# Performance work log

Measured on AMD Instinct MI355X. Metric: run time of the kernel, lower is better.

The kernel has to match this reference:

```python
import jax, jax.numpy as jnp
import numpy as np

D_MODEL = 768
N_HEAD = 12


def setup_inputs() -> dict:
    key = jax.random.key(0)
    k1, k2, k3, k4, k5 = jax.random.split(key, 5)
    B, T, C = 4, 2048, D_MODEL
    s = 1.0 / np.sqrt(C)
    return {
        "x": jax.random.normal(k1, (B, T, C), dtype=jnp.float32),
        "w_attn": jax.random.normal(k2, (C, 3 * C), dtype=jnp.float32) * s,
        "b_attn": jax.random.normal(k3, (3 * C,), dtype=jnp.float32) * 0.02,
        "w_proj": jax.random.normal(k4, (C, C), dtype=jnp.float32) * s,
        "b_proj": jax.random.normal(k5, (C,), dtype=jnp.float32) * 0.02,
    }


def reference(x, w_attn, b_attn, w_proj, b_proj):
    B, T, C = x.shape
    H = N_HEAD
    Dh = C // H
    qkv = x @ w_attn + b_attn                      # [B, T, 3C]
    q, k, v = jnp.split(qkv, 3, axis=-1)
    # [B, H, T, Dh]
    q = q.reshape(B, T, H, Dh).transpose(0, 2, 1, 3)
    k = k.reshape(B, T, H, Dh).transpose(0, 2, 1, 3)
    v = v.reshape(B, T, H, Dh).transpose(0, 2, 1, 3)
    att = jnp.einsum("bhqd,bhkd->bhqk", q, k) * (1.0 / np.sqrt(Dh))
    causal = jnp.tril(jnp.ones((T, T), dtype=bool))
    att = jnp.where(causal[None, None, :, :], att, -jnp.inf)
    att = jax.nn.softmax(att, axis=-1)             # dropout p=0 (eval)
    y = jnp.einsum("bhqk,bhkd->bhqd", att, v)      # [B, H, T, Dh]
    y = y.transpose(0, 2, 1, 3).reshape(B, T, C)
    return y @ w_proj + b_proj
```

## Files before the change

### kernel.cpp

```cpp
#include <hip/hip_runtime.h>
#include <stdint.h>

#define NHEAD 12
#define DH 64
#define BATCH 4
#define SEQ 2048
#define CDIM 768
#define MROWS (BATCH*SEQ)

typedef __attribute__((ext_vector_type(8))) short short8;
typedef __attribute__((ext_vector_type(4))) float floatx4;
typedef unsigned int u32;

__device__ inline unsigned short f2bf(float f) {
    union { float f; unsigned u; } v; v.f = f;
    unsigned r = v.u + 0x7FFFu + ((v.u >> 16) & 1u);
    return (unsigned short)(r >> 16);
}

__device__ __forceinline__ u32 pk_bf16(float a, float b) {
    u32 d;
    asm("v_cvt_pk_bf16_f32 %0, %1, %2" : "=v"(d) : "v"(a), "v"(b));
    return d;
}

__device__ __forceinline__ void async_cp16(const unsigned short* g, unsigned short* l) {
    __builtin_amdgcn_global_load_lds(
        (const __attribute__((address_space(1))) u32*)g,
        (__attribute__((address_space(3))) u32*)l, 16, 0, 0);
}

__global__ void convert_f32_bf16(const float* __restrict__ in,
                                 unsigned short* __restrict__ out, int n) {
    int i = (blockIdx.x * blockDim.x + threadIdx.x) * 4;
    if (i + 3 < n) {
        float4 f = *(const float4*)(in + i);
        union { unsigned short s[4]; uint2 u; } p;
        p.s[0] = f2bf(f.x); p.s[1] = f2bf(f.y);
        p.s[2] = f2bf(f.z); p.s[3] = f2bf(f.w);
        *(uint2*)(out + i) = p.u;
    }
}

__global__ __launch_bounds__(256) void transpose_conv(
    const float* __restrict__ in, unsigned short* __restrict__ out,
    int K, int N) {
    __shared__ unsigned short T[64][72];
    const int k0 = blockIdx.x * 64, n0 = blockIdx.y * 64;
    const int t = threadIdx.x;
    const int nc = t & 63, kw = t >> 6;
    for (int i = 0; i < 16; i++) {
        const int kr = kw + i * 4;
        T[nc][kr] = f2bf(in[(size_t)(k0 + kr) * N + n0 + nc]);
    }
    __syncthreads();
    const int row = t >> 2, seg = t & 3;
    uint4 a = *(const uint4*)&T[row][seg * 16];
    uint4 b2 = *(const uint4*)&T[row][seg * 16 + 8];
    unsigned short* o = &out[(size_t)(n0 + row) * K + k0 + seg * 16];
    *(uint4*)o = a;
    *(uint4*)(o + 8) = b2;
}

template<int MODE>
__global__ __launch_bounds__(256) void gemm_bf16(
    const unsigned short* __restrict__ A,
    const unsigned short* __restrict__ BT,
    const float* __restrict__ bias,
    float* __restrict__ Cout,
    unsigned short* __restrict__ Qout,
    unsigned short* __restrict__ Kout,
    unsigned short* __restrict__ VTout,
    int Ndim, int Kdim)
{
    __shared__ unsigned short As[2][128 * 32];
    __shared__ unsigned short Bs[2][128 * 32];
    const int tid  = threadIdx.x;
    const int wave = tid >> 6;
    const int lane = tid & 63;
    const int l16  = lane & 15;
    const int quad = lane >> 4;
    const int wm = wave >> 1, wn = wave & 1;
    const int m0 = blockIdx.x * 128;
    const int n0 = blockIdx.y * 128;

    const int rloc = lane >> 2;
    const int gs   = ((lane & 3) ^ (rloc & 3) ^ ((rloc >> 2) & 3)) * 8;
    const int ar0  = wave * 32 + rloc;
    const int pg = ((quad ^ (l16 & 3) ^ ((l16 >> 2) & 3))) * 8;

    floatx4 acc[4][4];
    for (int i = 0; i < 4; i++)
        for (int j = 0; j < 4; j++) acc[i][j] = (floatx4)0.0f;

    for (int ch = 0; ch < 2; ch++) {
        const int row = ar0 + ch * 16;
        async_cp16(&A[(size_t)(m0 + row) * Kdim + gs], &As[0][(wave * 2 + ch) * 512]);
        async_cp16(&BT[(size_t)(n0 + row) * Kdim + gs], &Bs[0][(wave * 2 + ch) * 512]);
    }
    __syncthreads();

    for (int k0 = 0; k0 < Kdim; k0 += 32) {
        const int cur = (k0 >> 5) & 1;
        if (k0 + 32 < Kdim) {
            for (int ch = 0; ch < 2; ch++) {
                const int row = ar0 + ch * 16;
                async_cp16(&A[(size_t)(m0 + row) * Kdim + k0 + 32 + gs],
                           &As[cur ^ 1][(wave * 2 + ch) * 512]);
                async_cp16(&BT[(size_t)(n0 + row) * Kdim + k0 + 32 + gs],
                           &Bs[cur ^ 1][(wave * 2 + ch) * 512]);
            }
        }
        short8 a[4], b[4];
        for (int i = 0; i < 4; i++)
            a[i] = *(const short8*)&As[cur][(wm * 64 + i * 16 + l16) * 32 + pg];
        for (int j = 0; j < 4; j++)
            b[j] = *(const short8*)&Bs[cur][(wn * 64 + j * 16 + l16) * 32 + pg];
        for (int i = 0; i < 4; i++)
            for (int j = 0; j < 4; j++)
                acc[i][j] = __builtin_amdgcn_mfma_f32_16x16x32_bf16(
                    a[i], b[j], acc[i][j], 0, 0, 0);
        __syncthreads();
    }

    const float QSCALE = 0.18033688011112042f;
    for (int i = 0; i < 4; i++) {
        const int mbase = m0 + wm * 64 + i * 16 + quad * 4;
        for (int j = 0; j < 4; j++) {
            const int ncol = n0 + wn * 64 + j * 16 + l16;
            const float bv = bias[ncol];
            for (int r = 0; r < 4; r++) {
                const int m = mbase + r;
                const float v = acc[i][j][r] + bv;
                if (MODE == 0) {
                    Cout[(size_t)m * Ndim + ncol] = v;
                } else {
                    const int b_  = m >> 11, t = m & 2047;
                    const int part = ncol / CDIM;
                    const int c = ncol - part * CDIM;
                    const int h = c >> 6, d = c & 63;
                    const size_t bh = (size_t)(b_ * NHEAD + h);
                    if (part == 0)
                        Qout[(bh * SEQ + t) * DH + d] = f2bf(v * QSCALE);
                    else if (part == 1)
                        Kout[(bh * SEQ + t) * DH + d] = f2bf(v);
                    else
                        VTout[(bh * DH + d) * SEQ + t] = f2bf(v);
                }
            }
        }
    }
}

__global__ __launch_bounds__(256) void attn_kernel(
    const unsigned short* __restrict__ Q,
    const unsigned short* __restrict__ K,
    const unsigned short* __restrict__ VT,
    unsigned short* __restrict__ O)
{
    __shared__ unsigned short Kl[2][2][64 * 32];
    __shared__ unsigned short Vl[2][2][64 * 32];
    __shared__ unsigned short Pl[4][16 * 68];

    const int tid  = threadIdx.x;
    const int wave = tid >> 6;
    const int lane = tid & 63;
    const int l16  = lane & 15;
    const int quad = lane >> 4;

    const int lin = blockIdx.x;
    const int grp = lin >> 3;
    const int xs  = grp & 15;
    const int bh  = ((grp >> 4) << 3) | (lin & 7);
    const int h = bh % NHEAD, b = bh / NHEAD;

    const unsigned short* Qp = Q  + (size_t)bh * SEQ * DH;
    const unsigned short* Kp = K  + (size_t)bh * SEQ * DH;
    const unsigned short* Vp = VT + (size_t)bh * DH * SEQ;

    const int rloc = lane >> 2;
    const int gofsK = ((lane & 3) ^ (rloc & 3) ^ ((rloc >> 2) & 3)) * 8;
    const int pg = ((quad ^ (l16 & 3) ^ ((l16 >> 2) & 3))) * 8;

    for (int pass = 0; pass < 2; pass++) {
        const int qtile = pass == 0 ? xs : 31 - xs;
        const int qb = qtile * 64;
        const int qw = qb + wave * 16;
        const int nkt = qtile + 1;

        short8 aq[2];
        for (int c = 0; c < 2; c++)
            aq[c] = *(const short8*)&Qp[(size_t)(qw + l16) * DH + c * 32 + quad * 8];

        floatx4 accO[4];
        for (int dt = 0; dt < 4; dt++) accO[dt] = (floatx4)0.0f;
        float lp = 0.0f;

        {
            const int krow = wave * 16 + rloc;
            for (int c = 0; c < 2; c++) {
                async_cp16(&Kp[(size_t)krow * DH + c * 32 + gofsK],
                           &Kl[0][c][wave * 512]);
                async_cp16(&Vp[(size_t)krow * SEQ + 0 + c * 32 + gofsK],
                           &Vl[0][c][wave * 512]);
            }
        }
        __syncthreads();

        for (int kt = 0; kt < nkt; kt++) {
            const int kb  = kt * 64;
            const int cur = kt & 1;

            if (kt + 1 < nkt) {
                const int kbn = kb + 64;
                const int krow = wave * 16 + rloc;
                for (int c = 0; c < 2; c++) {
                    async_cp16(&Kp[(size_t)(kbn + krow) * DH + c * 32 + gofsK],
                               &Kl[cur ^ 1][c][wave * 512]);
                    async_cp16(&Vp[(size_t)krow * SEQ + kbn + c * 32 + gofsK],
                               &Vl[cur ^ 1][c][wave * 512]);
                }
            }

            floatx4 s[4];
            for (int jn = 0; jn < 4; jn++) {
                s[jn] = (floatx4)0.0f;
                for (int c = 0; c < 2; c++) {
                    short8 bk = *(const short8*)
                        &Kl[cur][c][(jn * 16 + l16) * 32 + pg];
                    s[jn] = __builtin_amdgcn_mfma_f32_16x16x32_bf16(
                        bk, aq[c], s[jn], 0, 0, 0);
                }
            }

            if (kt == nkt - 1) {
                const int q = qw + l16;
                for (int jn = 0; jn < 4; jn++) {
                    const int key = kb + jn * 16 + quad * 4;
                    for (int r = 0; r < 4; r++)
                        if (key + r > q) s[jn][r] = -1e30f;
                }
            }

            for (int jn = 0; jn < 4; jn++)
                for (int r = 0; r < 4; r++) {
                    float p = exp2f(s[jn][r]);
                    s[jn][r] = p;
                    lp += p;
                }

            for (int jn = 0; jn < 4; jn++) {
                uint2 u;
                u.x = pk_bf16(s[jn][0], s[jn][1]);
                u.y = pk_bf16(s[jn][2], s[jn][3]);
                *(uint2*)&Pl[wave][l16 * 68 + jn * 16 + quad * 4] = u;
            }
            short8 ap[2];
            for (int c = 0; c < 2; c++) {
                union { short8 v; uint2 u2[2]; } a_;
                const int base = l16 * 68 + c * 32 + quad * 8;
                a_.u2[0] = *(const uint2*)&Pl[wave][base];
                a_.u2[1] = *(const uint2*)&Pl[wave][base + 4];
                ap[c] = a_.v;
            }

            for (int dt = 0; dt < 4; dt++)
                for (int c = 0; c < 2; c++) {
                    short8 bv = *(const short8*)
                        &Vl[cur][c][(dt * 16 + l16) * 32 + pg];
                    accO[dt] = __builtin_amdgcn_mfma_f32_16x16x32_bf16(
                        ap[c], bv, accO[dt], 0, 0, 0);
                }

            __syncthreads();
        }

        float L = lp;
        L += __shfl_xor(L, 16);
        L += __shfl_xor(L, 32);
        for (int r = 0; r < 4; r++) {
            const float Lr = __shfl(L, (lane & 48) | (quad * 4 + r), 64);
            const float inv = 1.0f / Lr;
            const int t = qb + wave * 16 + quad * 4 + r;
            const size_t base = ((size_t)b * SEQ + t) * CDIM + h * DH;
            for (int dt = 0; dt < 4; dt++)
                O[base + dt * 16 + l16] = f2bf(accO[dt][r] * inv);
        }
        __syncthreads();
    }
}

extern "C" void kernel_launch(void* const* d_in, const int* in_sizes, int n_in,
                              void* d_out, int out_size, void* d_ws, size_t ws_size,
                              hipStream_t stream) {
    const float* x      = (const float*)d_in[0];
    const float* w_attn = (const float*)d_in[1];
    const float* b_attn = (const float*)d_in[2];
    const float* w_proj = (const float*)d_in[3];
    const float* b_proj = (const float*)d_in[4];
    float* out = (float*)d_out;

    unsigned short* xb   = (unsigned short*)d_ws;
    unsigned short* wta  = xb  + (size_t)MROWS * CDIM;
    unsigned short* wtp  = wta + (size_t)3 * CDIM * CDIM;
    unsigned short* qws  = wtp + (size_t)CDIM * CDIM;
    unsigned short* kws  = qws + (size_t)MROWS * CDIM;
    unsigned short* vtws = kws + (size_t)MROWS * CDIM;
    unsigned short* ob   = xb;

    const int nx = MROWS * CDIM;
    convert_f32_bf16<<<nx / 1024, 256, 0, stream>>>(x, xb, nx);
    transpose_conv<<<dim3(CDIM / 64, 3 * CDIM / 64), 256, 0, stream>>>(
        w_attn, wta, CDIM, 3 * CDIM);
    transpose_conv<<<dim3(CDIM / 64, CDIM / 64), 256, 0, stream>>>(
        w_proj, wtp, CDIM, CDIM);

    dim3 g1(MROWS / 128, (3 * CDIM) / 128);
    gemm_bf16<1><<<g1, 256, 0, stream>>>(xb, wta, b_attn, nullptr,
                                         qws, kws, vtws, 3 * CDIM, CDIM);

    attn_kernel<<<768, 256, 0, stream>>>(qws, kws, vtws, ob);

    dim3 g3(MROWS / 128, CDIM / 128);
    gemm_bf16<0><<<g3, 256, 0, stream>>>(ob, wtp, b_proj, out,
                                         nullptr, nullptr, nullptr, CDIM, CDIM);
}
```

Measured before the change: 223.2 us.

## Split attention keys across waves and triple-buffer GEMM loads with vmcnt waits

The attention kernel now has each wave process all 64 query rows of a tile against a strided subset of 32-key blocks, loading K and V straight from global memory into registers instead of staging them in LDS. Partial outputs and row sums are then reduced through shared memory at the end of each pass, which removes the per-tile block barriers. The GEMM moves to a compile-time K dimension and a three-stage LDS ring that waits with s_waitcnt vmcnt and a bare s_barrier, and the epilogue index math is hoisted out of the inner loop. The trade-off is more register pressure from 16 accumulator tiles per wave (with launch bounds set to 2 blocks), uncoalesced direct global loads, and an extra cross-wave reduction.

```diff
diff --git a/kernel.cpp b/kernel.cpp
--- a/kernel.cpp
+++ b/kernel.cpp
@@ -62,7 +62,7 @@
     *(uint4*)(o + 8) = b2;
 }
 
-template<int MODE>
+template<int MODE, int KD>
 __global__ __launch_bounds__(256) void gemm_bf16(
     const unsigned short* __restrict__ A,
     const unsigned short* __restrict__ BT,
@@ -71,10 +71,10 @@
     unsigned short* __restrict__ Qout,
     unsigned short* __restrict__ Kout,
     unsigned short* __restrict__ VTout,
-    int Ndim, int Kdim)
+    int Ndim)
 {
-    __shared__ unsigned short As[2][128 * 32];
-    __shared__ unsigned short Bs[2][128 * 32];
+    __shared__ unsigned short As[3][4096];
+    __shared__ unsigned short Bs[3][4096];
     const int tid  = threadIdx.x;
     const int wave = tid >> 6;
     const int lane = tid & 63;
@@ -85,7 +85,7 @@
     const int n0 = blockIdx.y * 128;
 
     const int rloc = lane >> 2;
-    const int gs   = ((lane & 3) ^ (rloc & 3) ^ ((rloc >> 2) & 3)) * 8;
+    const int gs   = (((lane & 3) ^ (rloc & 3) ^ ((rloc >> 2) & 3))) * 8;
     const int ar0  = wave * 32 + rloc;
     const int pg = ((quad ^ (l16 & 3) ^ ((l16 >> 2) & 3))) * 8;
 
@@ -93,53 +93,61 @@
     for (int i = 0; i < 4; i++)
         for (int j = 0; j < 4; j++) acc[i][j] = (floatx4)0.0f;
 
-    for (int ch = 0; ch < 2; ch++) {
-        const int row = ar0 + ch * 16;
-        async_cp16(&A[(size_t)(m0 + row) * Kdim + gs], &As[0][(wave * 2 + ch) * 512]);
-        async_cp16(&BT[(size_t)(n0 + row) * Kdim + gs], &Bs[0][(wave * 2 + ch) * 512]);
-    }
-    __syncthreads();
-
-    for (int k0 = 0; k0 < Kdim; k0 += 32) {
-        const int cur = (k0 >> 5) & 1;
-        if (k0 + 32 < Kdim) {
-            for (int ch = 0; ch < 2; ch++) {
-                const int row = ar0 + ch * 16;
-                async_cp16(&A[(size_t)(m0 + row) * Kdim + k0 + 32 + gs],
-                           &As[cur ^ 1][(wave * 2 + ch) * 512]);
-                async_cp16(&BT[(size_t)(n0 + row) * Kdim + k0 + 32 + gs],
-                           &Bs[cur ^ 1][(wave * 2 + ch) * 512]);
-            }
+    constexpr int NIT = KD / 32;
+
+    auto stageTo = [&](int s, int buf) {
+        const int koff = s * 32;
+        for (int ch = 0; ch < 2; ch++) {
+            const int row = ar0 + ch * 16;
+            async_cp16(&A[(size_t)(m0 + row) * KD + koff + gs],
+                       &As[buf][(wave * 2 + ch) * 512]);
+            async_cp16(&BT[(size_t)(n0 + row) * KD + koff + gs],
+                       &Bs[buf][(wave * 2 + ch) * 512]);
+        }
+    };
+    stageTo(0, 0);
+    stageTo(1, 1);
+
+    int buf = 0;
+    for (int it = 0; it < NIT; it++) {
+        if (it < NIT - 1) asm volatile("s_waitcnt vmcnt(4)" ::: "memory");
+        else              asm volatile("s_waitcnt vmcnt(0)" ::: "memory");
+        asm volatile("s_barrier" ::: "memory");
+        if (it + 2 < NIT) {
+            int b2 = buf + 2; if (b2 >= 3) b2 -= 3;
+            stageTo(it + 2, b2);
         }
         short8 a[4], b[4];
         for (int i = 0; i < 4; i++)
-            a[i] = *(const short8*)&As[cur][(wm * 64 + i * 16 + l16) * 32 + pg];
+            a[i] = *(const short8*)&As[buf][(wm * 64 + i * 16 + l16) * 32 + pg];
         for (int j = 0; j < 4; j++)
-            b[j] = *(const short8*)&Bs[cur][(wn * 64 + j * 16 + l16) * 32 + pg];
+            b[j] = *(const short8*)&Bs[buf][(wn * 64 + j * 16 + l16) * 32 + pg];
         for (int i = 0; i < 4; i++)
             for (int j = 0; j < 4; j++)
                 acc[i][j] = __builtin_amdgcn_mfma_f32_16x16x32_bf16(
                     a[i], b[j], acc[i][j], 0, 0, 0);
-        __syncthreads();
+        buf++; if (buf >= 3) buf = 0;
     }
 
     const float QSCALE = 0.18033688011112042f;
     for (int i = 0; i < 4; i++) {
         const int mbase = m0 + wm * 64 + i * 16 + quad * 4;
         for (int j = 0; j < 4; j++) {
-            const int ncol = n0 + wn * 64 + j * 16 + l16;
+            const int ncj  = n0 + wn * 64 + j * 16;
+            const int part = ncj / CDIM;
+            const int cj   = ncj - part * CDIM;
+            const int ncol = ncj + l16;
             const float bv = bias[ncol];
+            const int c = cj + l16;
+            const int hh = c >> 6, d = c & 63;
             for (int r = 0; r < 4; r++) {
                 const int m = mbase + r;
                 const float v = acc[i][j][r] + bv;
                 if (MODE == 0) {
                     Cout[(size_t)m * Ndim + ncol] = v;
                 } else {
-                    const int b_  = m >> 11, t = m & 2047;
-                    const int part = ncol / CDIM;
-                    const int c = ncol - part * CDIM;
-                    const int h = c >> 6, d = c & 63;
-                    const size_t bh = (size_t)(b_ * NHEAD + h);
+                    const int b_ = m >> 11, t = m & 2047;
+                    const size_t bh = (size_t)(b_ * NHEAD + hh);
                     if (part == 0)
                         Qout[(bh * SEQ + t) * DH + d] = f2bf(v * QSCALE);
                     else if (part == 1)
@@ -152,15 +160,15 @@
     }
 }
 
-__global__ __launch_bounds__(256) void attn_kernel(
+__global__ __launch_bounds__(256, 2) void attn_kernel(
     const unsigned short* __restrict__ Q,
     const unsigned short* __restrict__ K,
     const unsigned short* __restrict__ VT,
     unsigned short* __restrict__ O)
 {
-    __shared__ unsigned short Kl[2][2][64 * 32];
-    __shared__ unsigned short Vl[2][2][64 * 32];
-    __shared__ unsigned short Pl[4][16 * 68];
+    __shared__ float MO[4 * 3 * 4 * 256];
+    __shared__ float ML[4][4][16];
+    __shared__ unsigned short Pl[4][16 * 40];
 
     const int tid  = threadIdx.x;
     const int wave = tid >> 6;
@@ -178,113 +186,124 @@
     const unsigned short* Kp = K  + (size_t)bh * SEQ * DH;
     const unsigned short* Vp = VT + (size_t)bh * DH * SEQ;
 
-    const int rloc = lane >> 2;
-    const int gofsK = ((lane & 3) ^ (rloc & 3) ^ ((rloc >> 2) & 3)) * 8;
-    const int pg = ((quad ^ (l16 & 3) ^ ((l16 >> 2) & 3))) * 8;
-
     for (int pass = 0; pass < 2; pass++) {
         const int qtile = pass == 0 ? xs : 31 - xs;
-        const int qb = qtile * 64;
-        const int qw = qb + wave * 16;
-        const int nkt = qtile + 1;
-
-        short8 aq[2];
-        for (int c = 0; c < 2; c++)
-            aq[c] = *(const short8*)&Qp[(size_t)(qw + l16) * DH + c * 32 + quad * 8];
-
-        floatx4 accO[4];
-        for (int dt = 0; dt < 4; dt++) accO[dt] = (floatx4)0.0f;
-        float lp = 0.0f;
-
+        const int qb  = qtile * 64;
+        const int nkt = 2 * (qtile + 1);
+
+        short8 aq[4][2];
+        for (int qi = 0; qi < 4; qi++)
+            for (int c = 0; c < 2; c++)
+                aq[qi][c] = *(const short8*)
+                    &Qp[(size_t)(qb + qi * 16 + l16) * DH + c * 32 + quad * 8];
+
+        floatx4 accO[4][4];
+        for (int qi = 0; qi < 4; qi++)
+            for (int dt = 0; dt < 4; dt++) accO[qi][dt] = (floatx4)0.0f;
+        float lp[4] = {0.f, 0.f, 0.f, 0.f};
+
+        int kt = pass == 0 ? wave : 3 - wave;
+        short8 bkC[2][2], bkN[2][2], bv[4];
+        if (kt < nkt) {
+            const int kb = kt * 32;
+            for (int jn = 0; jn < 2; jn++)
+                for (int c = 0; c < 2; c++)
+                    bkC[jn][c] = *(const short8*)
+                        &Kp[(size_t)(kb + jn * 16 + l16) * DH + c * 32 + quad * 8];
+        }
+
+        for (; kt < nkt; kt += 4) {
+            const int kb = kt * 32;
+            const bool havN = (kt + 4 < nkt);
+            if (havN) {
+                const int kbn = kb + 128;
+                for (int jn = 0; jn < 2; jn++)
+                    for (int c = 0; c < 2; c++)
+                        bkN[jn][c] = *(const short8*)
+                            &Kp[(size_t)(kbn + jn * 16 + l16) * DH + c * 32 + quad * 8];
+            }
+            for (int dt = 0; dt < 4; dt++)
+                bv[dt] = *(const short8*)
+                    &Vp[(size_t)(dt * 16 + l16) * SEQ + kb + quad * 8];
+
+            floatx4 s[4][2];
+            for (int qi = 0; qi < 4; qi++)
+                for (int jn = 0; jn < 2; jn++) {
+                    floatx4 t0 = __builtin_amdgcn_mfma_f32_16x16x32_bf16(
+                        bkC[jn][0], aq[qi][0], (floatx4)0.0f, 0, 0, 0);
+                    s[qi][jn] = __builtin_amdgcn_mfma_f32_16x16x32_bf16(
+                        bkC[jn][1], aq[qi][1], t0, 0, 0, 0);
+                }
+            if (havN)
+                for (int jn = 0; jn < 2; jn++)
+                    for (int c = 0; c < 2; c++) bkC[jn][c] = bkN[jn][c];
+
+            for (int qi = 0; qi < 4; qi++) {
+                const int qlo = qb + qi * 16;
+                if (kb > qlo + 15) continue;
+                if (kb + 31 > qlo) {
+                    const int q = qlo + l16;
+                    for (int jn = 0; jn < 2; jn++) {
+                        const int key = kb + jn * 16 + quad * 4;
+                        for (int r = 0; r < 4; r++)
+                            if (key + r > q) s[qi][jn][r] = -1e30f;
+                    }
+                }
+                float sum = lp[qi];
+                for (int jn = 0; jn < 2; jn++)
+                    for (int r = 0; r < 4; r++) {
+                        float p = exp2f(s[qi][jn][r]);
+                        s[qi][jn][r] = p;
+                        sum += p;
+                    }
+                lp[qi] = sum;
+
+                for (int jn = 0; jn < 2; jn++) {
+                    uint2 u;
+                    u.x = pk_bf16(s[qi][jn][0], s[qi][jn][1]);
+                    u.y = pk_bf16(s[qi][jn][2], s[qi][jn][3]);
+                    *(uint2*)&Pl[wave][l16 * 40 + jn * 16 + quad * 4] = u;
+                }
+                short8 ap = *(const short8*)&Pl[wave][l16 * 40 + quad * 8];
+                for (int dt = 0; dt < 4; dt++)
+                    accO[qi][dt] = __builtin_amdgcn_mfma_f32_16x16x32_bf16(
+                        ap, bv[dt], accO[qi][dt], 0, 0, 0);
+            }
+        }
+
+        for (int qi = 0; qi < 4; qi++) {
+            if (qi == wave) continue;
+            const int slot = (wave > qi) ? wave - 1 : wave;
+            for (int dt = 0; dt < 4; dt++)
+                *(floatx4*)&MO[(((qi * 3 + slot) * 4 + dt) << 8) + lane * 4] =
+                    accO[qi][dt];
+        }
+        for (int qi = 0; qi < 4; qi++) {
+            float Lq = lp[qi];
+            Lq += __shfl_xor(Lq, 16);
+            Lq += __shfl_xor(Lq, 32);
+            if (quad == 0) ML[qi][wave][l16] = Lq;
+        }
+        __syncthreads();
         {
-            const int krow = wave * 16 + rloc;
-            for (int c = 0; c < 2; c++) {
-                async_cp16(&Kp[(size_t)krow * DH + c * 32 + gofsK],
-                           &Kl[0][c][wave * 512]);
-                async_cp16(&Vp[(size_t)krow * SEQ + 0 + c * 32 + gofsK],
-                           &Vl[0][c][wave * 512]);
-            }
-        }
-        __syncthreads();
-
-        for (int kt = 0; kt < nkt; kt++) {
-            const int kb  = kt * 64;
-            const int cur = kt & 1;
-
-            if (kt + 1 < nkt) {
-                const int kbn = kb + 64;
-                const int krow = wave * 16 + rloc;
-                for (int c = 0; c < 2; c++) {
-                    async_cp16(&Kp[(size_t)(kbn + krow) * DH + c * 32 + gofsK],
-                               &Kl[cur ^ 1][c][wave * 512]);
-                    async_cp16(&Vp[(size_t)krow * SEQ + kbn + c * 32 + gofsK],
-                               &Vl[cur ^ 1][c][wave * 512]);
-                }
-            }
-
-            floatx4 s[4];
-            for (int jn = 0; jn < 4; jn++) {
-                s[jn] = (floatx4)0.0f;
-                for (int c = 0; c < 2; c++) {
-                    short8 bk = *(const short8*)
-                        &Kl[cur][c][(jn * 16 + l16) * 32 + pg];
-                    s[jn] = __builtin_amdgcn_mfma_f32_16x16x32_bf16(
-                        bk, aq[c], s[jn], 0, 0, 0);
-                }
-            }
-
-            if (kt == nkt - 1) {
-                const int q = qw + l16;
-                for (int jn = 0; jn < 4; jn++) {
-                    const int key = kb + jn * 16 + quad * 4;
-                    for (int r = 0; r < 4; r++)
-                        if (key + r > q) s[jn][r] = -1e30f;
-                }
-            }
-
-            for (int jn = 0; jn < 4; jn++)
-                for (int r = 0; r < 4; r++) {
-                    float p = exp2f(s[jn][r]);
-                    s[jn][r] = p;
-                    lp += p;
-                }
-
-            for (int jn = 0; jn < 4; jn++) {
-                uint2 u;
-                u.x = pk_bf16(s[jn][0], s[jn][1]);
-                u.y = pk_bf16(s[jn][2], s[jn][3]);
-                *(uint2*)&Pl[wave][l16 * 68 + jn * 16 + quad * 4] = u;
-            }
-            short8 ap[2];
-            for (int c = 0; c < 2; c++) {
-                union { short8 v; uint2 u2[2]; } a_;
-                const int base = l16 * 68 + c * 32 + quad * 8;
-                a_.u2[0] = *(const uint2*)&Pl[wave][base];
-                a_.u2[1] = *(const uint2*)&Pl[wave][base + 4];
-                ap[c] = a_.v;
-            }
-
-            for (int dt = 0; dt < 4; dt++)
-                for (int c = 0; c < 2; c++) {
-                    short8 bv = *(const short8*)
-                        &Vl[cur][c][(dt * 16 + l16) * 32 + pg];
-                    accO[dt] = __builtin_amdgcn_mfma_f32_16x16x32_bf16(
-                        ap[c], bv, accO[dt], 0, 0, 0);
-                }
-
-            __syncthreads();
-        }
-
-        float L = lp;
-        L += __shfl_xor(L, 16);
-        L += __shfl_xor(L, 32);
-        for (int r = 0; r < 4; r++) {
-            const float Lr = __shfl(L, (lane & 48) | (quad * 4 + r), 64);
-            const float inv = 1.0f / Lr;
-            const int t = qb + wave * 16 + quad * 4 + r;
-            const size_t base = ((size_t)b * SEQ + t) * CDIM + h * DH;
-            for (int dt = 0; dt < 4; dt++)
-                O[base + dt * 16 + l16] = f2bf(accO[dt][r] * inv);
+            const int qi = wave;
+            floatx4 o[4];
+            for (int dt = 0; dt < 4; dt++) {
+                o[dt] = accO[qi][dt];
+                for (int slot = 0; slot < 3; slot++)
+                    o[dt] += *(const floatx4*)
+                        &MO[(((qi * 3 + slot) * 4 + dt) << 8) + lane * 4];
+            }
+            const float Ls = ML[qi][0][l16] + ML[qi][1][l16] +
+                             ML[qi][2][l16] + ML[qi][3][l16];
+            for (int r = 0; r < 4; r++) {
+                const float Lr = __shfl(Ls, quad * 4 + r, 64);
+                const float inv = 1.0f / Lr;
+                const int t = qb + wave * 16 + quad * 4 + r;
+                const size_t base = ((size_t)b * SEQ + t) * CDIM + h * DH;
+                for (int dt = 0; dt < 4; dt++)
+                    O[base + dt * 16 + l16] = f2bf(o[dt][r] * inv);
+            }
         }
         __syncthreads();
     }
@@ -316,12 +335,12 @@
         w_proj, wtp, CDIM, CDIM);
 
     dim3 g1(MROWS / 128, (3 * CDIM) / 128);
-    gemm_bf16<1><<<g1, 256, 0, stream>>>(xb, wta, b_attn, nullptr,
-                                         qws, kws, vtws, 3 * CDIM, CDIM);
+    gemm_bf16<1, CDIM><<<g1, 256, 0, stream>>>(xb, wta, b_attn, nullptr,
+                                               qws, kws, vtws, 3 * CDIM);
 
     attn_kernel<<<768, 256, 0, stream>>>(qws, kws, vtws, ob);
 
     dim3 g3(MROWS / 128, CDIM / 128);
-    gemm_bf16<0><<<g3, 256, 0, stream>>>(ob, wtp, b_proj, out,
-                                         nullptr, nullptr, nullptr, CDIM, CDIM);
-}
+    gemm_bf16<0, CDIM><<<g3, 256, 0, stream>>>(ob, wtp, b_proj, out,
+                                               nullptr, nullptr, nullptr, CDIM);
+}
```

Result: slower. 316.7 us (+41.9%).
